# Kernel optimization log

Measured on AMD Instinct MI355X. Metric: run time of the kernel, lower is better.

## Reference

```python
import jax, jax.numpy as jnp
import numpy as np

N, E = 20000, 320000
NODE_DIM, HID, HEADS, OUT = 256, 64, 4, 50
NEG_SLOPE = 0.2  # PyG GATv2Conv default
BN_EPS = 1e-5


def setup_inputs() -> dict:
    key = jax.random.key(0)
    ks = jax.random.split(key, 16)
    s = 0.05
    inp = {
        'x': jax.random.normal(ks[0], (N, NODE_DIM), dtype=jnp.float32),
        'edge_index': jax.random.randint(ks[1], (2, E), 0, N, dtype=jnp.int64),
        # GATv2 layer 1: in=NODE_DIM, out=HID, heads=HEADS, concat
        'W1l': jax.random.normal(ks[2], (NODE_DIM, HEADS * HID), dtype=jnp.float32) * s,
        'W1r': jax.random.normal(ks[3], (NODE_DIM, HEADS * HID), dtype=jnp.float32) * s,
        'att1': jax.random.normal(ks[4], (HEADS, HID), dtype=jnp.float32) * s,
        'b1': jnp.zeros((HEADS * HID,), dtype=jnp.float32),
        'bn1_g': jnp.ones((HEADS * HID,), dtype=jnp.float32),
        'bn1_b': jnp.zeros((HEADS * HID,), dtype=jnp.float32),
        # GATv2 layer 2: in=HEADS*HID, out=HID, heads=1
        'W2l': jax.random.normal(ks[5], (HEADS * HID, HID), dtype=jnp.float32) * s,
        'W2r': jax.random.normal(ks[6], (HEADS * HID, HID), dtype=jnp.float32) * s,
        'att2': jax.random.normal(ks[7], (1, HID), dtype=jnp.float32) * s,
        'b2': jnp.zeros((HID,), dtype=jnp.float32),
        'bn2_g': jnp.ones((HID,), dtype=jnp.float32),
        'bn2_b': jnp.zeros((HID,), dtype=jnp.float32),
        # class head
        'Wc': jax.random.normal(ks[8], (HID, OUT), dtype=jnp.float32) * s,
        'bc': jnp.zeros((OUT,), dtype=jnp.float32),
    }
    return inp


def gatv2(x, src, dst, Wl, Wr, att, bias, heads, d):
    n = x.shape[0]
    xl = (x @ Wl).reshape(n, heads, d)  # source-side transform (messages)
    xr = (x @ Wr).reshape(n, heads, d)  # target-side transform
    xj = xl[src]                        # [E, H, D] gathered source feats
    xi = xr[dst]                        # [E, H, D] gathered target feats
    e = jax.nn.leaky_relu(xi + xj, NEG_SLOPE)
    score = jnp.einsum('ehd,hd->eh', e, att)   # [E, H]
    # segment softmax over incoming edges of each destination node
    m = jax.ops.segment_max(score, dst, num_segments=n)         # [N, H]
    m = jnp.where(jnp.isfinite(m), m, 0.0)
    p = jnp.exp(score - m[dst])
    denom = jax.ops.segment_sum(p, dst, num_segments=n)          # [N, H]
    alpha = p / (denom[dst] + 1e-16)
    out = jax.ops.segment_sum(alpha[:, :, None] * xj, dst, num_segments=n)  # [N, H, D]
    return out.reshape(n, heads * d) + bias


def batchnorm(x, gamma, beta):
    mu = jnp.mean(x, axis=0)
    var = jnp.var(x, axis=0)
    return (x - mu) * jax.lax.rsqrt(var + BN_EPS) * gamma + beta


def reference(x, edge_index, W1l, W1r, att1, b1, bn1_g, bn1_b,
              W2l, W2r, att2, b2, bn2_g, bn2_b, Wc, bc):
    src, dst = edge_index[0], edge_index[1]
    h = gatv2(x, src, dst, W1l, W1r, att1, b1, HEADS, HID)
    h = jax.nn.gelu(batchnorm(h, bn1_g, bn1_b), approximate=False)
    h = gatv2(h, src, dst, W2l, W2r, att2, b2, 1, HID)
    h = jax.nn.gelu(batchnorm(h, bn2_g, bn2_b), approximate=False)
    return jax.nn.log_softmax(h @ Wc + bc, axis=1)
```

## Files before the change

### kernel.cpp

```cpp
#include <hip/hip_runtime.h>
#include <math.h>

#define N_NODES 20000
#define N_EDGES 320000
#define NODE_DIM 256
#define HID 64
#define HEADS 4
#define OUTC 50
#define NEG_SLOPE 0.2f
#define BN_EPS 1e-5f
#define LOG2E 1.4426950408889634f

typedef __attribute__((ext_vector_type(8))) short short8;
typedef __attribute__((ext_vector_type(8))) unsigned short ushort8;
typedef __attribute__((ext_vector_type(4))) unsigned short ushort4v;
typedef __attribute__((ext_vector_type(4))) float f32x4;

__device__ inline unsigned short f2bf(float f) {
  unsigned u = __float_as_uint(f);
  u += 0x7fffu + ((u >> 16) & 1u);
  return (unsigned short)(u >> 16);
}

__device__ inline float bf2f(unsigned short u) {
  return __uint_as_float((unsigned)u << 16);
}

__device__ inline float gelu_exact(float v) {
  return 0.5f * v * (1.f + erff(v * 0.70710678118f));
}

__global__ void cast_all_kernel(const float* __restrict__ x, unsigned short* __restrict__ xb,
                                const float* __restrict__ W1l, const float* __restrict__ W1r,
                                const float* __restrict__ W2l, const float* __restrict__ W2r,
                                unsigned short* __restrict__ w1bT,
                                unsigned short* __restrict__ w2bT,
                                const int* __restrict__ dst, int* __restrict__ deg) {
  int i = blockIdx.x * blockDim.x + threadIdx.x;
  if (i < 1280000) {
    float4 v = ((const float4*)x)[i];
    ushort4v o = {f2bf(v.x), f2bf(v.y), f2bf(v.z), f2bf(v.w)};
    ((ushort4v*)xb)[i] = o;
  }
  if (i < 131072) {
    int j = i >> 8, k = i & 255;
    w1bT[i] = f2bf(j < 256 ? W1l[k * 256 + j] : W1r[k * 256 + j - 256]);
  }
  if (i < 32768) {
    int j = i >> 8, k = i & 255;
    w2bT[i] = f2bf(j < 64 ? W2l[k * 64 + j] : W2r[k * 64 + j - 64]);
  }
  if (i < N_EDGES) atomicAdd(&deg[dst[i]], 1);
}

__global__ void scan_kernel(const int* __restrict__ deg, int* __restrict__ rowptr,
                            int* __restrict__ cursor) {
  __shared__ int part[1024];
  int tid = threadIdx.x;
  const int CH = (N_NODES + 1023) / 1024;
  int base = tid * CH;
  int s = 0;
#pragma unroll
  for (int i = 0; i < CH; i++) {
    int idx = base + i;
    if (idx < N_NODES) s += deg[idx];
  }
  part[tid] = s;
  __syncthreads();
  for (int off = 1; off < 1024; off <<= 1) {
    int v = (tid >= off) ? part[tid - off] : 0;
    __syncthreads();
    part[tid] += v;
    __syncthreads();
  }
  int run = (tid == 0) ? 0 : part[tid - 1];
#pragma unroll
  for (int i = 0; i < CH; i++) {
    int idx = base + i;
    if (idx < N_NODES) {
      rowptr[idx] = run;
      cursor[idx] = 0;
      run += deg[idx];
    }
  }
  if (tid == 1023) rowptr[N_NODES] = run;
}

__global__ __launch_bounds__(256) void gemm_bf16_kernel(
    const unsigned short* __restrict__ A, const unsigned short* __restrict__ BT,
    unsigned short* __restrict__ C, int M, int K, int N) {
  __shared__ unsigned short As[128][40];
  __shared__ unsigned short Bs[128][40];
  int tid = threadIdx.x;
  int lane = tid & 63, w = tid >> 6;
  int bm = blockIdx.y * 128, bn = blockIdx.x * 128;

  f32x4 acc[2][8] = {};

  for (int k0 = 0; k0 < K; k0 += 32) {
#pragma unroll
    for (int s = tid; s < 512; s += 256) {
      int row = s >> 2, half = s & 3;
      int gr = bm + row;
      ushort8 v = {0, 0, 0, 0, 0, 0, 0, 0};
      if (gr < M) v = *(const ushort8*)&A[(size_t)gr * K + k0 + half * 8];
      *(ushort8*)&As[row][half * 8] = v;
    }
#pragma unroll
    for (int s = tid; s < 512; s += 256) {
      int row = s >> 2, half = s & 3;
      ushort8 v = *(const ushort8*)&BT[(size_t)(bn + row) * K + k0 + half * 8];
      *(ushort8*)&Bs[row][half * 8] = v;
    }
    __syncthreads();

    short8 av[2], bv[8];
#pragma unroll
    for (int fr = 0; fr < 2; fr++)
      av[fr] = *(const short8*)&As[w * 32 + fr * 16 + (lane & 15)][(lane >> 4) * 8];
#pragma unroll
    for (int fc = 0; fc < 8; fc++)
      bv[fc] = *(const short8*)&Bs[fc * 16 + (lane & 15)][(lane >> 4) * 8];
#pragma unroll
    for (int fr = 0; fr < 2; fr++)
#pragma unroll
      for (int fc = 0; fc < 8; fc++)
        acc[fr][fc] = __builtin_amdgcn_mfma_f32_16x16x32_bf16(av[fr], bv[fc], acc[fr][fc], 0, 0, 0);
    __syncthreads();
  }

#pragma unroll
  for (int fr = 0; fr < 2; fr++)
#pragma unroll
    for (int fc = 0; fc < 8; fc++)
#pragma unroll
      for (int i = 0; i < 4; i++) {
        int r = bm + w * 32 + fr * 16 + (lane >> 4) * 4 + i;
        if (r < M) C[(size_t)r * N + bn + fc * 16 + (lane & 15)] = f2bf(acc[fr][fc][i]);
      }
}

__global__ __launch_bounds__(256) void gemm2_fused_kernel(
    const unsigned short* __restrict__ Ab, const float* __restrict__ ss,
    const unsigned short* __restrict__ BT, unsigned short* __restrict__ C,
    int M, int K, int N) {
  __shared__ unsigned short As[128][40];
  __shared__ unsigned short Bs[128][40];
  __shared__ float ssA[512];
  int tid = threadIdx.x;
  int lane = tid & 63, w = tid >> 6;
  int bm = blockIdx.y * 128, bn = blockIdx.x * 128;

  for (int i = tid; i < 512; i += 256) ssA[i] = ss[i];
  __syncthreads();

  f32x4 acc[2][8] = {};

  for (int k0 = 0; k0 < K; k0 += 32) {
#pragma unroll
    for (int s = tid; s < 512; s += 256) {
      int row = s >> 2, half = s & 3;
      int gr = bm + row;
      int c0 = k0 + half * 8;
      ushort8 o8 = {0, 0, 0, 0, 0, 0, 0, 0};
      if (gr < M) {
        ushort8 raw = *(const ushort8*)&Ab[(size_t)gr * K + c0];
#pragma unroll
        for (int j = 0; j < 8; j++)
          o8[j] = f2bf(gelu_exact(bf2f(raw[j]) * ssA[c0 + j] + ssA[256 + c0 + j]));
      }
      *(ushort8*)&As[row][half * 8] = o8;
    }
#pragma unroll
    for (int s = tid; s < 512; s += 256) {
      int row = s >> 2, half = s & 3;
      ushort8 v = *(const ushort8*)&BT[(size_t)(bn + row) * K + k0 + half * 8];
      *(ushort8*)&Bs[row][half * 8] = v;
    }
    __syncthreads();

    short8 av[2], bv[8];
#pragma unroll
    for (int fr = 0; fr < 2; fr++)
      av[fr] = *(const short8*)&As[w * 32 + fr * 16 + (lane & 15)][(lane >> 4) * 8];
#pragma unroll
    for (int fc = 0; fc < 8; fc++)
      bv[fc] = *(const short8*)&Bs[fc * 16 + (lane & 15)][(lane >> 4) * 8];
#pragma unroll
    for (int fr = 0; fr < 2; fr++)
#pragma unroll
      for (int fc = 0; fc < 8; fc++)
        acc[fr][fc] = __builtin_amdgcn_mfma_f32_16x16x32_bf16(av[fr], bv[fc], acc[fr][fc], 0, 0, 0);
    __syncthreads();
  }

#pragma unroll
  for (int fr = 0; fr < 2; fr++)
#pragma unroll
    for (int fc = 0; fc < 8; fc++)
#pragma unroll
      for (int i = 0; i < 4; i++) {
        int r = bm + w * 32 + fr * 16 + (lane >> 4) * 4 + i;
        if (r < M) C[(size_t)r * N + bn + fc * 16 + (lane & 15)] = f2bf(acc[fr][fc][i]);
      }
}

__global__ void scatter_kernel(const int* __restrict__ src, const int* __restrict__ dst,
                               const int* __restrict__ rowptr, int* __restrict__ cursor,
                               int* __restrict__ csr_src) {
  int i = blockIdx.x * blockDim.x + threadIdx.x;
  if (i < N_EDGES) {
    int d = dst[i];
    int pos = rowptr[d] + atomicAdd(&cursor[d], 1);
    csr_src[pos] = src[i];
  }
}

__global__ void agg1_kernel(const unsigned short* __restrict__ C1,
                            const float* __restrict__ att, const float* __restrict__ bias,
                            const int* __restrict__ rowptr, const int* __restrict__ csr_src,
                            unsigned short* __restrict__ out) {
  int wave = threadIdx.x >> 6;
  int lane = threadIdx.x & 63;
  int n = blockIdx.x * 4 + wave;
  if (n >= N_NODES) return;

  ushort4v xi4 = *(const ushort4v*)&C1[(size_t)n * 512 + 256 + 4 * lane];
  float xi0 = bf2f(xi4[0]), xi1 = bf2f(xi4[1]), xi2 = bf2f(xi4[2]), xi3 = bf2f(xi4[3]);
  float4 attv = *(const float4*)&att[4 * lane];
  attv.x *= LOG2E; attv.y *= LOG2E; attv.z *= LOG2E; attv.w *= LOG2E;

  float acc0 = 0.f, acc1 = 0.f, acc2 = 0.f, acc3 = 0.f;
  float lsum = 0.f;

  int e0 = rowptr[n], e1 = rowptr[n + 1];
  int e = e0;
#define EDGE_SCORE(T, X0, X1, X2, X3)                                                 \
  {                                                                                   \
    float u0 = xi0 + X0, u1 = xi1 + X1, u2 = xi2 + X2, u3 = xi3 + X3;                 \
    T = fmaxf(u0, NEG_SLOPE * u0) * attv.x + fmaxf(u1, NEG_SLOPE * u1) * attv.y +     \
        fmaxf(u2, NEG_SLOPE * u2) * attv.z + fmaxf(u3, NEG_SLOPE * u3) * attv.w;      \
  }
  for (; e + 4 <= e1; e += 4) {
    int s0 = csr_src[e], s1 = csr_src[e + 1], s2 = csr_src[e + 2], s3 = csr_src[e + 3];
    ushort4v a4 = *(const ushort4v*)&C1[(size_t)s0 * 512 + 4 * lane];
    ushort4v b4 = *(const ushort4v*)&C1[(size_t)s1 * 512 + 4 * lane];
    ushort4v c4 = *(const ushort4v*)&C1[(size_t)s2 * 512 + 4 * lane];
    ushort4v d4 = *(const ushort4v*)&C1[(size_t)s3 * 512 + 4 * lane];
    float xa0 = bf2f(a4[0]), xa1 = bf2f(a4[1]), xa2 = bf2f(a4[2]), xa3 = bf2f(a4[3]);
    float xb0 = bf2f(b4[0]), xb1 = bf2f(b4[1]), xb2 = bf2f(b4[2]), xb3 = bf2f(b4[3]);
    float xc0 = bf2f(c4[0]), xc1 = bf2f(c4[1]), xc2 = bf2f(c4[2]), xc3 = bf2f(c4[3]);
    float xd0 = bf2f(d4[0]), xd1 = bf2f(d4[1]), xd2 = bf2f(d4[2]), xd3 = bf2f(d4[3]);

    float ta, tb, tc, td;
    EDGE_SCORE(ta, xa0, xa1, xa2, xa3);
    EDGE_SCORE(tb, xb0, xb1, xb2, xb3);
    EDGE_SCORE(tc, xc0, xc1, xc2, xc3);
    EDGE_SCORE(td, xd0, xd1, xd2, xd3);

    ta += __shfl_xor(ta, 8); tb += __shfl_xor(tb, 8); tc += __shfl_xor(tc, 8); td += __shfl_xor(td, 8);
    ta += __shfl_xor(ta, 4); tb += __shfl_xor(tb, 4); tc += __shfl_xor(tc, 4); td += __shfl_xor(td, 4);
    ta += __shfl_xor(ta, 2); tb += __shfl_xor(tb, 2); tc += __shfl_xor(tc, 2); td += __shfl_xor(td, 2);
    ta += __shfl_xor(ta, 1); tb += __shfl_xor(tb, 1); tc += __shfl_xor(tc, 1); td += __shfl_xor(td, 1);

    float pa = __builtin_amdgcn_exp2f(ta);
    float pb = __builtin_amdgcn_exp2f(tb);
    float pc = __builtin_amdgcn_exp2f(tc);
    float pd = __builtin_amdgcn_exp2f(td);
    lsum += (pa + pb) + (pc + pd);
    acc0 += pa * xa0 + pb * xb0 + pc * xc0 + pd * xd0;
    acc1 += pa * xa1 + pb * xb1 + pc * xc1 + pd * xd1;
    acc2 += pa * xa2 + pb * xb2 + pc * xc2 + pd * xd2;
    acc3 += pa * xa3 + pb * xb3 + pc * xc3 + pd * xd3;
  }
  for (; e < e1; e++) {
    int s0 = csr_src[e];
    ushort4v a4 = *(const ushort4v*)&C1[(size_t)s0 * 512 + 4 * lane];
    float xa0 = bf2f(a4[0]), xa1 = bf2f(a4[1]), xa2 = bf2f(a4[2]), xa3 = bf2f(a4[3]);
    float ta;
    EDGE_SCORE(ta, xa0, xa1, xa2, xa3);
    ta += __shfl_xor(ta, 8);
    ta += __shfl_xor(ta, 4);
    ta += __shfl_xor(ta, 2);
    ta += __shfl_xor(ta, 1);
    float pa = __builtin_amdgcn_exp2f(ta);
    lsum += pa;
    acc0 += pa * xa0;
    acc1 += pa * xa1;
    acc2 += pa * xa2;
    acc3 += pa * xa3;
  }
#undef EDGE_SCORE

  float inv = 1.f / (lsum + 1e-16f);
  float4 bv = *(const float4*)&bias[4 * lane];
  ushort4v o = {f2bf(acc0 * inv + bv.x), f2bf(acc1 * inv + bv.y),
                f2bf(acc2 * inv + bv.z), f2bf(acc3 * inv + bv.w)};
  *(ushort4v*)&out[(size_t)n * 256 + 4 * lane] = o;
}

__global__ void agg2_kernel(const unsigned short* __restrict__ xlr,
                            const float* __restrict__ att, const float* __restrict__ bias,
                            const int* __restrict__ rowptr, const int* __restrict__ csr_src,
                            float* __restrict__ out) {
  int wave = threadIdx.x >> 6;
  int lane = threadIdx.x & 63;
  int n = blockIdx.x * 4 + wave;
  if (n >= N_NODES) return;

  int g = lane >> 4, slot = lane & 15;
  ushort4v xi4 = *(const ushort4v*)&xlr[(size_t)n * 128 + 64 + 4 * slot];
  float xi0 = bf2f(xi4[0]), xi1 = bf2f(xi4[1]), xi2 = bf2f(xi4[2]), xi3 = bf2f(xi4[3]);
  float4 attv = *(const float4*)&att[4 * slot];
  attv.x *= LOG2E; attv.y *= LOG2E; attv.z *= LOG2E; attv.w *= LOG2E;

  float acc0 = 0.f, acc1 = 0.f, acc2 = 0.f, acc3 = 0.f;
  float lsum = 0.f;

  int e0 = rowptr[n], e1 = rowptr[n + 1];
  int nt = (e1 - e0 + 3) >> 2;
  for (int it = 0; it < nt; it++) {
    int e = e0 + it * 4 + g;
    bool valid = e < e1;
    int s = valid ? csr_src[e] : 0;
    ushort4v xj4 = *(const ushort4v*)&xlr[(size_t)s * 128 + 4 * slot];
    float xj0 = bf2f(xj4[0]), xj1 = bf2f(xj4[1]), xj2 = bf2f(xj4[2]), xj3 = bf2f(xj4[3]);
    float u0 = xi0 + xj0, u1 = xi1 + xj1, u2 = xi2 + xj2, u3 = xi3 + xj3;
    float t = fmaxf(u0, NEG_SLOPE * u0) * attv.x + fmaxf(u1, NEG_SLOPE * u1) * attv.y +
              fmaxf(u2, NEG_SLOPE * u2) * attv.z + fmaxf(u3, NEG_SLOPE * u3) * attv.w;
    t += __shfl_xor(t, 8);
    t += __shfl_xor(t, 4);
    t += __shfl_xor(t, 2);
    t += __shfl_xor(t, 1);
    float p = valid ? __builtin_amdgcn_exp2f(t) : 0.f;
    lsum += p;
    acc0 += p * xj0;
    acc1 += p * xj1;
    acc2 += p * xj2;
    acc3 += p * xj3;
  }

  acc0 += __shfl_xor(acc0, 16); acc0 += __shfl_xor(acc0, 32);
  acc1 += __shfl_xor(acc1, 16); acc1 += __shfl_xor(acc1, 32);
  acc2 += __shfl_xor(acc2, 16); acc2 += __shfl_xor(acc2, 32);
  acc3 += __shfl_xor(acc3, 16); acc3 += __shfl_xor(acc3, 32);
  lsum += __shfl_xor(lsum, 16); lsum += __shfl_xor(lsum, 32);

  if (g == 0) {
    float inv = 1.f / (lsum + 1e-16f);
    float4 bv = *(const float4*)&bias[4 * slot];
    float4 o;
    o.x = acc0 * inv + bv.x;
    o.y = acc1 * inv + bv.y;
    o.z = acc2 * inv + bv.z;
    o.w = acc3 * inv + bv.w;
    *(float4*)&out[(size_t)n * 64 + 4 * slot] = o;
  }
}

__global__ void bn_stage1_256_kernel(const unsigned short* __restrict__ x,
                                     float* __restrict__ partial) {
  int c = threadIdx.x;
  int r0 = blockIdx.x * 84;
  int r1 = min(r0 + 84, N_NODES);
  float s = 0.f, q = 0.f;
  for (int r = r0; r < r1; r++) {
    float v = bf2f(x[(size_t)r * 256 + c]);
    s += v;
    q += v * v;
  }
  partial[(size_t)blockIdx.x * 512 + c] = s;
  partial[(size_t)blockIdx.x * 512 + 256 + c] = q;
}

__global__ void bn_stage1_64_kernel(const float* __restrict__ x, float* __restrict__ partial) {
  __shared__ float ls[256], lq[256];
  int tid = threadIdx.x;
  int c = tid & 63, g = tid >> 6;
  int r0 = blockIdx.x * 84 + g;
  int r1 = min(blockIdx.x * 84 + 84, N_NODES);
  float s = 0.f, q = 0.f;
  for (int r = r0; r < r1; r += 4) {
    float v = x[(size_t)r * 64 + c];
    s += v;
    q += v * v;
  }
  ls[tid] = s;
  lq[tid] = q;
  __syncthreads();
  if (g == 0) {
    s += ls[64 + c] + ls[128 + c] + ls[192 + c];
    q += lq[64 + c] + lq[128 + c] + lq[192 + c];
    partial[(size_t)blockIdx.x * 128 + c] = s;
    partial[(size_t)blockIdx.x * 128 + 64 + c] = q;
  }
}

__global__ void bn_stage2_kernel(const float* __restrict__ partial, int C,
                                 const float* __restrict__ gamma, const float* __restrict__ beta,
                                 float* __restrict__ ss) {
  int c = threadIdx.x;
  if (c >= C) return;
  float s = 0.f, q = 0.f;
  for (int b = 0; b < 240; b++) {
    s += partial[(size_t)b * 2 * C + c];
    q += partial[(size_t)b * 2 * C + C + c];
  }
  float mu = s * (1.0f / N_NODES);
  float var = q * (1.0f / N_NODES) - mu * mu;
  float sc = gamma[c] * rsqrtf(var + BN_EPS);
  ss[c] = sc;
  ss[C + c] = beta[c] - mu * sc;
}

__global__ void head_kernel(const float* __restrict__ h, const float* __restrict__ ss2,
                            const float* __restrict__ Wc, const float* __restrict__ bc,
                            float* __restrict__ out) {
  __shared__ float Ws[HID * OUTC];
  __shared__ float bs[OUTC];
  for (int i = threadIdx.x; i < HID * OUTC; i += 256) Ws[i] = Wc[i];
  for (int i = threadIdx.x; i < OUTC; i += 256) bs[i] = bc[i];
  __syncthreads();

  int wave = threadIdx.x >> 6;
  int lane = threadIdx.x & 63;
  int n = blockIdx.x * 4 + wave;
  if (n >= N_NODES) return;

  float raw = h[(size_t)n * HID + lane];
  float hrow = gelu_exact(raw * ss2[lane] + ss2[64 + lane]);
  float dot = 0.f;
#pragma unroll
  for (int k = 0; k < HID; k++) {
    float hk = __shfl(hrow, k);
    if (lane < OUTC) dot += hk * Ws[k * OUTC + lane];
  }
  float z = (lane < OUTC) ? (dot + bs[lane]) : -INFINITY;
  float mv = z;
  for (int off = 32; off; off >>= 1) mv = fmaxf(mv, __shfl_xor(mv, off));
  float p = (lane < OUTC) ? expf(z - mv) : 0.f;
  float sum = p;
  for (int off = 32; off; off >>= 1) sum += __shfl_xor(sum, off);
  if (lane < OUTC) out[(size_t)n * OUTC + lane] = z - mv - logf(sum);
}

extern "C" void kernel_launch(void* const* d_in, const int* in_sizes, int n_in,
                              void* d_out, int out_size, void* d_ws, size_t ws_size,
                              hipStream_t stream) {
  const float* x = (const float*)d_in[0];
  const int* eidx = (const int*)d_in[1];
  const float* W1l = (const float*)d_in[2];
  const float* W1r = (const float*)d_in[3];
  const float* att1 = (const float*)d_in[4];
  const float* b1 = (const float*)d_in[5];
  const float* bn1_g = (const float*)d_in[6];
  const float* bn1_b = (const float*)d_in[7];
  const float* W2l = (const float*)d_in[8];
  const float* W2r = (const float*)d_in[9];
  const float* att2 = (const float*)d_in[10];
  const float* b2 = (const float*)d_in[11];
  const float* bn2_g = (const float*)d_in[12];
  const float* bn2_b = (const float*)d_in[13];
  const float* Wc = (const float*)d_in[14];
  const float* bc = (const float*)d_in[15];
  float* out = (float*)d_out;

  const int* src = eidx;
  const int* dstv = eidx + N_EDGES;

  char* ws = (char*)d_ws;
  unsigned short* C1full = (unsigned short*)(ws + 0);
  unsigned short* out1b = (unsigned short*)(ws + 20971520);
  unsigned short* C2full = (unsigned short*)(ws + 52428800);
  unsigned short* xb = (unsigned short*)(ws + 62914560);
  float* out2 = (float*)(ws + 62914560);
  float* partial = (float*)(ws + 73400320);
  float* ss1 = (float*)(ws + 73891840);
  float* ss2 = (float*)(ws + 73893888);
  unsigned short* w1bT = (unsigned short*)(ws + 73894400);
  unsigned short* w2bT = (unsigned short*)(ws + 74156544);
  int* deg = (int*)(ws + 74222080);
  int* cursor = (int*)(ws + 74302080);
  int* rowptr = (int*)(ws + 74382080);
  int* csr_src = (int*)(ws + 74462096);

  hipMemsetAsync(deg, 0, 80000, stream);

  cast_all_kernel<<<5000, 256, 0, stream>>>(x, xb, W1l, W1r, W2l, W2r, w1bT, w2bT, dstv, deg);

  scan_kernel<<<1, 1024, 0, stream>>>(deg, rowptr, cursor);

  gemm_bf16_kernel<<<dim3(4, 157), 256, 0, stream>>>(xb, w1bT, C1full, N_NODES, 256, 512);

  scatter_kernel<<<(N_EDGES + 255) / 256, 256, 0, stream>>>(src, dstv, rowptr, cursor, csr_src);

  agg1_kernel<<<N_NODES / 4, 256, 0, stream>>>(C1full, att1, b1, rowptr, csr_src, out1b);

  bn_stage1_256_kernel<<<240, 256, 0, stream>>>(out1b, partial);
  bn_stage2_kernel<<<1, 256, 0, stream>>>(partial, 256, bn1_g, bn1_b, ss1);

  gemm2_fused_kernel<<<dim3(1, 157), 256, 0, stream>>>(out1b, ss1, w2bT, C2full, N_NODES, 256, 128);

  agg2_kernel<<<N_NODES / 4, 256, 0, stream>>>(C2full, att2, b2, rowptr, csr_src, out2);

  bn_stage1_64_kernel<<<240, 256, 0, stream>>>(out2, partial);
  bn_stage2_kernel<<<1, 64, 0, stream>>>(partial, 64, bn2_g, bn2_b, ss2);

  head_kernel<<<N_NODES / 4, 256, 0, stream>>>(out2, ss2, Wc, bc, out);
}
```

Measured before the change: 265.4 us.

## Fuse edge scatter into layer-1 GEMM launch and widen GEMM K-tile to 64

The CSR scatter now runs as extra blocks inside the layer-1 GEMM launch, using a flattened 1D grid, so the two independent stages share one launch and can overlap. Both GEMM kernels now stage 64-wide K slices in LDS with an inner two-step MFMA loop, which halves the number of barrier-separated iterations. The trade-off is larger LDS per block, which may lower occupancy. The scatter blocks also share the grid with the GEMM tiles and may compete with them for resources.

```diff
diff --git a/kernel.cpp b/kernel.cpp
--- a/kernel.cpp
+++ b/kernel.cpp
@@ -88,44 +88,62 @@
 
 __global__ __launch_bounds__(256) void gemm_bf16_kernel(
     const unsigned short* __restrict__ A, const unsigned short* __restrict__ BT,
-    unsigned short* __restrict__ C, int M, int K, int N) {
-  __shared__ unsigned short As[128][40];
-  __shared__ unsigned short Bs[128][40];
+    unsigned short* __restrict__ C, int M, int K, int N, int gemmBlocks,
+    const int* __restrict__ src, const int* __restrict__ dst,
+    const int* __restrict__ rowptr, int* __restrict__ cursor,
+    int* __restrict__ csr_src) {
+  int b = blockIdx.x;
+  if (b >= gemmBlocks) {
+    int i = (b - gemmBlocks) * 256 + threadIdx.x;
+    if (i < N_EDGES) {
+      int d = dst[i];
+      int pos = rowptr[d] + atomicAdd(&cursor[d], 1);
+      csr_src[pos] = src[i];
+    }
+    return;
+  }
+
+  __shared__ unsigned short As[128][72];
+  __shared__ unsigned short Bs[128][72];
   int tid = threadIdx.x;
   int lane = tid & 63, w = tid >> 6;
-  int bm = blockIdx.y * 128, bn = blockIdx.x * 128;
+  int nbx = N >> 7;
+  int bm = (b / nbx) * 128, bn = (b % nbx) * 128;
 
   f32x4 acc[2][8] = {};
 
-  for (int k0 = 0; k0 < K; k0 += 32) {
-#pragma unroll
-    for (int s = tid; s < 512; s += 256) {
-      int row = s >> 2, half = s & 3;
+  for (int k0 = 0; k0 < K; k0 += 64) {
+#pragma unroll
+    for (int s = tid; s < 1024; s += 256) {
+      int row = s >> 3, half = s & 7;
       int gr = bm + row;
       ushort8 v = {0, 0, 0, 0, 0, 0, 0, 0};
       if (gr < M) v = *(const ushort8*)&A[(size_t)gr * K + k0 + half * 8];
       *(ushort8*)&As[row][half * 8] = v;
     }
 #pragma unroll
-    for (int s = tid; s < 512; s += 256) {
-      int row = s >> 2, half = s & 3;
+    for (int s = tid; s < 1024; s += 256) {
+      int row = s >> 3, half = s & 7;
       ushort8 v = *(const ushort8*)&BT[(size_t)(bn + row) * K + k0 + half * 8];
       *(ushort8*)&Bs[row][half * 8] = v;
     }
     __syncthreads();
 
-    short8 av[2], bv[8];
-#pragma unroll
-    for (int fr = 0; fr < 2; fr++)
-      av[fr] = *(const short8*)&As[w * 32 + fr * 16 + (lane & 15)][(lane >> 4) * 8];
-#pragma unroll
-    for (int fc = 0; fc < 8; fc++)
-      bv[fc] = *(const short8*)&Bs[fc * 16 + (lane & 15)][(lane >> 4) * 8];
-#pragma unroll
-    for (int fr = 0; fr < 2; fr++)
+#pragma unroll
+    for (int kk = 0; kk < 2; kk++) {
+      short8 av[2], bv[8];
+#pragma unroll
+      for (int fr = 0; fr < 2; fr++)
+        av[fr] = *(const short8*)&As[w * 32 + fr * 16 + (lane & 15)][kk * 32 + (lane >> 4) * 8];
 #pragma unroll
       for (int fc = 0; fc < 8; fc++)
-        acc[fr][fc] = __builtin_amdgcn_mfma_f32_16x16x32_bf16(av[fr], bv[fc], acc[fr][fc], 0, 0, 0);
+        bv[fc] = *(const short8*)&Bs[fc * 16 + (lane & 15)][kk * 32 + (lane >> 4) * 8];
+#pragma unroll
+      for (int fr = 0; fr < 2; fr++)
+#pragma unroll
+        for (int fc = 0; fc < 8; fc++)
+          acc[fr][fc] = __builtin_amdgcn_mfma_f32_16x16x32_bf16(av[fr], bv[fc], acc[fr][fc], 0, 0, 0);
+    }
     __syncthreads();
   }
 
@@ -144,22 +162,23 @@
     const unsigned short* __restrict__ Ab, const float* __restrict__ ss,
     const unsigned short* __restrict__ BT, unsigned short* __restrict__ C,
     int M, int K, int N) {
-  __shared__ unsigned short As[128][40];
-  __shared__ unsigned short Bs[128][40];
+  __shared__ unsigned short As[128][72];
+  __shared__ unsigned short Bs[128][72];
   __shared__ float ssA[512];
   int tid = threadIdx.x;
   int lane = tid & 63, w = tid >> 6;
-  int bm = blockIdx.y * 128, bn = blockIdx.x * 128;
+  int nbx = N >> 7;
+  int bm = ((int)blockIdx.x / nbx) * 128, bn = ((int)blockIdx.x % nbx) * 128;
 
   for (int i = tid; i < 512; i += 256) ssA[i] = ss[i];
   __syncthreads();
 
   f32x4 acc[2][8] = {};
 
-  for (int k0 = 0; k0 < K; k0 += 32) {
-#pragma unroll
-    for (int s = tid; s < 512; s += 256) {
-      int row = s >> 2, half = s & 3;
+  for (int k0 = 0; k0 < K; k0 += 64) {
+#pragma unroll
+    for (int s = tid; s < 1024; s += 256) {
+      int row = s >> 3, half = s & 7;
       int gr = bm + row;
       int c0 = k0 + half * 8;
       ushort8 o8 = {0, 0, 0, 0, 0, 0, 0, 0};
@@ -172,25 +191,28 @@
       *(ushort8*)&As[row][half * 8] = o8;
     }
 #pragma unroll
-    for (int s = tid; s < 512; s += 256) {
-      int row = s >> 2, half = s & 3;
+    for (int s = tid; s < 1024; s += 256) {
+      int row = s >> 3, half = s & 7;
       ushort8 v = *(const ushort8*)&BT[(size_t)(bn + row) * K + k0 + half * 8];
       *(ushort8*)&Bs[row][half * 8] = v;
     }
     __syncthreads();
 
-    short8 av[2], bv[8];
-#pragma unroll
-    for (int fr = 0; fr < 2; fr++)
-      av[fr] = *(const short8*)&As[w * 32 + fr * 16 + (lane & 15)][(lane >> 4) * 8];
-#pragma unroll
-    for (int fc = 0; fc < 8; fc++)
-      bv[fc] = *(const short8*)&Bs[fc * 16 + (lane & 15)][(lane >> 4) * 8];
-#pragma unroll
-    for (int fr = 0; fr < 2; fr++)
+#pragma unroll
+    for (int kk = 0; kk < 2; kk++) {
+      short8 av[2], bv[8];
+#pragma unroll
+      for (int fr = 0; fr < 2; fr++)
+        av[fr] = *(const short8*)&As[w * 32 + fr * 16 + (lane & 15)][kk * 32 + (lane >> 4) * 8];
 #pragma unroll
       for (int fc = 0; fc < 8; fc++)
-        acc[fr][fc] = __builtin_amdgcn_mfma_f32_16x16x32_bf16(av[fr], bv[fc], acc[fr][fc], 0, 0, 0);
+        bv[fc] = *(const short8*)&Bs[fc * 16 + (lane & 15)][kk * 32 + (lane >> 4) * 8];
+#pragma unroll
+      for (int fr = 0; fr < 2; fr++)
+#pragma unroll
+        for (int fc = 0; fc < 8; fc++)
+          acc[fr][fc] = __builtin_amdgcn_mfma_f32_16x16x32_bf16(av[fr], bv[fc], acc[fr][fc], 0, 0, 0);
+    }
     __syncthreads();
   }
 
@@ -203,17 +225,6 @@
         int r = bm + w * 32 + fr * 16 + (lane >> 4) * 4 + i;
         if (r < M) C[(size_t)r * N + bn + fc * 16 + (lane & 15)] = f2bf(acc[fr][fc][i]);
       }
-}
-
-__global__ void scatter_kernel(const int* __restrict__ src, const int* __restrict__ dst,
-                               const int* __restrict__ rowptr, int* __restrict__ cursor,
-                               int* __restrict__ csr_src) {
-  int i = blockIdx.x * blockDim.x + threadIdx.x;
-  if (i < N_EDGES) {
-    int d = dst[i];
-    int pos = rowptr[d] + atomicAdd(&cursor[d], 1);
-    csr_src[pos] = src[i];
-  }
 }
 
 __global__ void agg1_kernel(const unsigned short* __restrict__ C1,
@@ -490,16 +501,20 @@
 
   scan_kernel<<<1, 1024, 0, stream>>>(deg, rowptr, cursor);
 
-  gemm_bf16_kernel<<<dim3(4, 157), 256, 0, stream>>>(xb, w1bT, C1full, N_NODES, 256, 512);
-
-  scatter_kernel<<<(N_EDGES + 255) / 256, 256, 0, stream>>>(src, dstv, rowptr, cursor, csr_src);
+  {
+    const int gemmBlocks = 4 * 157;
+    const int scatBlocks = (N_EDGES + 255) / 256;
+    gemm_bf16_kernel<<<gemmBlocks + scatBlocks, 256, 0, stream>>>(
+        xb, w1bT, C1full, N_NODES, 256, 512, gemmBlocks,
+        src, dstv, rowptr, cursor, csr_src);
+  }
 
   agg1_kernel<<<N_NODES / 4, 256, 0, stream>>>(C1full, att1, b1, rowptr, csr_src, out1b);
 
   bn_stage1_256_kernel<<<240, 256, 0, stream>>>(out1b, partial);
   bn_stage2_kernel<<<1, 256, 0, stream>>>(partial, 256, bn1_g, bn1_b, ss1);
 
-  gemm2_fused_kernel<<<dim3(1, 157), 256, 0, stream>>>(out1b, ss1, w2bT, C2full, N_NODES, 256, 128);
+  gemm2_fused_kernel<<<157, 256, 0, stream>>>(out1b, ss1, w2bT, C2full, N_NODES, 256, 128);
 
   agg2_kernel<<<N_NODES / 4, 256, 0, stream>>>(C2full, att2, b2, rowptr, csr_src, out2);
 
```

Result: slower. 273.2 us (+2.9%).
